# Kernel tuning notes

Hardware: AMD Instinct MI355X
Metric: run time of the kernel (lower is better)

## Reference

```python
import jax, jax.numpy as jnp
import numpy as np

NUM_NODE = 50000
NUM_EDGE = 1_600_000
NUM_REL = 512
DIM = 64


def setup_inputs() -> dict:
    key = jax.random.key(0)
    k1, k2, k3, k4, k5, k6 = jax.random.split(key, 6)
    inp = jax.random.normal(k1, (NUM_NODE, DIM), dtype=jnp.float32)
    boundary = jax.random.normal(k2, (NUM_NODE, DIM), dtype=jnp.float32)
    node_in = jax.random.randint(k3, (NUM_EDGE,), 0, NUM_NODE)
    node_out = jax.random.randint(k4, (NUM_EDGE,), 0, NUM_NODE)
    rel = jax.random.randint(k5, (NUM_EDGE,), 0, NUM_REL)
    edge_list = jnp.stack([node_in, node_out, rel], axis=1).astype(jnp.int32)
    edge_weight = jnp.ones((NUM_EDGE,), dtype=jnp.float32)
    relation_weight = jax.random.normal(k6, (NUM_REL, DIM), dtype=jnp.float32)
    W = jax.random.normal(jax.random.fold_in(key, 7), (DIM, DIM), dtype=jnp.float32) / np.sqrt(DIM)
    b = jnp.zeros((DIM,), dtype=jnp.float32)
    return {"input": inp, "boundary": boundary, "edge_list": edge_list,
            "edge_weight": edge_weight, "relation_weight": relation_weight,
            "W": W, "b": b}


def reference(input, boundary, edge_list, edge_weight, relation_weight, W, b):
    node_in = edge_list[:, 0]
    node_out = edge_list[:, 1]
    rel = edge_list[:, 2]
    # message: DistMult = x_src * r_e   [E, D]
    msg = input[node_in] * relation_weight[rel]
    msg = msg * edge_weight[:, None]
    # std aggregation: sum and sq_sum scatters, boundary acts as an extra self-message
    s = jax.ops.segment_sum(msg, node_out, num_segments=NUM_NODE) + boundary
    sq = jax.ops.segment_sum(msg * msg, node_out, num_segments=NUM_NODE) + boundary * boundary
    deg = jax.ops.segment_sum(jnp.ones_like(edge_weight), node_out, num_segments=NUM_NODE)
    deg1 = (deg + 1.0)[:, None]  # degree_out + 1 (boundary counted)
    update = jnp.sqrt(jnp.clip(sq / deg1 - (s / deg1) ** 2, 1e-6))
    # add_model: single Linear (MLP with num_mlp_layer=1, no trailing activation)
    return update @ W.T + b
```

## Files before the change

### kernel.cpp

```cpp
#include <hip/hip_runtime.h>
#include <hip/hip_bf16.h>

#define NN  50000
#define NE  1600000
#define DIM 64
#define NBK 391

#define OFF_FLAGS  0
#define OFF_BOFF   8
#define OFF_BCUR   400
#define OFF_ROWPTR 792
#define OFF_EIDX   50800

#define CHUNK 4096
#define SBCAP 8192

typedef __bf16 bf16x8 __attribute__((ext_vector_type(8)));
typedef __bf16 bf16x4 __attribute__((ext_vector_type(4)));
typedef float  f32x4  __attribute__((ext_vector_type(4)));

__device__ __forceinline__ float loadF(const void* p, int i, int bf) {
  if (bf) return __bfloat162float(((const __hip_bfloat16*)p)[i]);
  return ((const float*)p)[i];
}

__device__ __forceinline__ float4 loadF4(const void* p, int i4, int bf) {
  if (bf) {
    ushort4 u = ((const ushort4*)p)[i4];
    float4 f;
    union { unsigned int ui; float fl; } c;
    c.ui = (unsigned int)u.x << 16; f.x = c.fl;
    c.ui = (unsigned int)u.y << 16; f.y = c.fl;
    c.ui = (unsigned int)u.z << 16; f.z = c.fl;
    c.ui = (unsigned int)u.w << 16; f.w = c.fl;
    return f;
  }
  return ((const float4*)p)[i4];
}

__global__ void k_detect(const void* input, const void* boundary,
                         const void* relw, const void* W, const void* ew,
                         int* flags, int* boff) {
  __shared__ int cnt;
  int t = threadIdx.x;
  const void* arrs[4] = {input, boundary, relw, W};
  for (int a = 0; a < 4; ++a) {
    if (t == 0) cnt = 0;
    __syncthreads();
    const unsigned short* u = (const unsigned short*)arrs[a];
    unsigned ex = (u[2 * t] >> 7) & 0xFF;
    if (ex >= 100 && ex <= 140) atomicAdd(&cnt, 1);
    __syncthreads();
    if (t == 0) flags[a] = (cnt >= 32) ? 1 : 0;
    __syncthreads();
  }
  if (t == 0) {
    flags[4] = (((const unsigned short*)ew)[0] == 0x3F80) ? 1 : 0;
    flags[5] = 1;
  }
  for (int i = t; i < 392; i += 64) boff[i] = 0;
}

__global__ __launch_bounds__(256) void k_bhist(const int* __restrict__ el,
                                               const void* __restrict__ ew,
                                               int* __restrict__ bcnt,
                                               int* __restrict__ flags) {
  __shared__ int lc[NBK];
  int t = threadIdx.x;
  int bfE = flags[4];
  for (int i = t; i < NBK; i += 256) lc[i] = 0;
  __syncthreads();
  int c0 = blockIdx.x * 8192;
  int bad = 0;
  for (int i = t; i < 8192; i += 256) {
    int e = c0 + i;
    if (e < NE) {
      atomicAdd(&lc[el[e * 3 + 1] >> 7], 1);
      if (loadF(ew, e, bfE) != 1.0f) bad = 1;
    }
  }
  if (bad) flags[5] = 0;
  __syncthreads();
  for (int i = t; i < NBK; i += 256)
    if (lc[i]) atomicAdd(&bcnt[i], lc[i]);
}

__global__ __launch_bounds__(256) void k_scanb(int* __restrict__ boff,
                                               int* __restrict__ bcur,
                                               int* __restrict__ rowptr) {
  __shared__ int sc[256];
  int t = threadIdx.x;
  int i0 = 2 * t, i1 = 2 * t + 1;
  int a = (i0 < 392) ? boff[i0] : 0;
  int b = (i1 < 392) ? boff[i1] : 0;
  sc[t] = a + b;
  __syncthreads();
  for (int off = 1; off < 256; off <<= 1) {
    int v = (t >= off) ? sc[t - off] : 0;
    __syncthreads();
    sc[t] += v;
    __syncthreads();
  }
  int excl = sc[t] - (a + b);
  if (i0 < 392) boff[i0] = excl;
  if (i1 < 392) boff[i1] = excl + a;
  if (i0 < NBK) bcur[i0] = excl;
  if (i1 < NBK) bcur[i1] = excl + a;
  if (t == 255) rowptr[NN] = sc[255];
}

__global__ __launch_bounds__(256) void k_parta(
    const int* __restrict__ el, int* __restrict__ bcur,
    int* __restrict__ eidx, const int* __restrict__ flags,
    const int* __restrict__ boff, int gb0, int gb1, int cap) {
  __shared__ int stage[CHUNK];
  __shared__ unsigned short sbk[CHUNK];
  __shared__ int lh[NBK], lbase[NBK], lh2[NBK], gbs[NBK];
  __shared__ int sc[256];
  __shared__ int total;
  int t = threadIdx.x;
  int nb = gb1 - gb0;
  int c0 = blockIdx.x * CHUNK;
  int ones = flags[5];
  int base0 = boff[gb0];
  for (int i = t; i < nb; i += 256) { lh[i] = 0; lh2[i] = 0; }
  __syncthreads();
  for (int i = t; i < CHUNK; i += 256) {
    int e = c0 + i;
    if (e < NE) {
      int b = (el[e * 3 + 1] >> 7) - gb0;
      if (b >= 0 && b < nb) atomicAdd(&lh[b], 1);
    }
  }
  __syncthreads();
  int a0 = (2 * t < nb) ? lh[2 * t] : 0;
  int a1 = (2 * t + 1 < nb) ? lh[2 * t + 1] : 0;
  sc[t] = a0 + a1;
  __syncthreads();
  for (int off = 1; off < 256; off <<= 1) {
    int v = (t >= off) ? sc[t - off] : 0;
    __syncthreads();
    sc[t] += v;
    __syncthreads();
  }
  int excl = sc[t] - (a0 + a1);
  if (2 * t < nb) {
    lbase[2 * t] = excl;
    if (a0 > 0) gbs[2 * t] = atomicAdd(&bcur[gb0 + 2 * t], a0);
  }
  if (2 * t + 1 < nb) {
    lbase[2 * t + 1] = excl + a0;
    if (a1 > 0) gbs[2 * t + 1] = atomicAdd(&bcur[gb0 + 2 * t + 1], a1);
  }
  if (t == 255) total = sc[255];
  __syncthreads();
  for (int i = t; i < CHUNK; i += 256) {
    int e = c0 + i;
    if (e < NE) {
      int nout = el[e * 3 + 1];
      int b = (nout >> 7) - gb0;
      if (b >= 0 && b < nb) {
        int r = atomicAdd(&lh2[b], 1);
        int slot = lbase[b] + r;
        int rec = ones ? (el[e * 3] | (el[e * 3 + 2] << 16) |
                          ((nout & 127) << 25))
                       : (e | ((nout & 127) << 25));
        stage[slot] = rec;
        sbk[slot] = (unsigned short)b;
      }
    }
  }
  __syncthreads();
  int tot = total;
  for (int i = t; i < tot; i += 256) {
    int b = sbk[i];
    int dst = gbs[b] + (i - lbase[b]) - base0;
    if (dst >= 0 && dst < cap) eidx[dst] = stage[i];
  }
}

__global__ __launch_bounds__(256) void k_partb(
    int* __restrict__ eidx, const int* __restrict__ boff,
    int* __restrict__ rowptr, const int* __restrict__ el,
    const int* __restrict__ flags, int gb0, int cap) {
  __shared__ int ld[SBCAP];
  __shared__ int lcnt[128], lexc[128];
  int t = threadIdx.x;
  int b = gb0 + blockIdx.x;
  int n0 = b * 128;
  int ncnt = min(128, NN - n0);
  int base0 = boff[gb0];
  int rbase = boff[b], rend = boff[b + 1];
  int cnt = rend - rbase;
  int fast = (cnt <= SBCAP) && (rend - base0 <= cap);
  if (t < 128) lcnt[t] = 0;
  __syncthreads();
  if (fast) {
    for (int i = t; i < cnt; i += 256) ld[i] = eidx[rbase - base0 + i];
    __syncthreads();
    for (int i = t; i < cnt; i += 256)
      atomicAdd(&lcnt[(((unsigned)ld[i]) >> 25) & 127], 1);
  } else {
    int lim = n0 + ncnt;
    for (int e = t; e < NE; e += 256) {
      int nout = el[e * 3 + 1];
      if (nout >= n0 && nout < lim) atomicAdd(&lcnt[nout - n0], 1);
    }
  }
  __syncthreads();
  if (t < 128) lexc[t] = lcnt[t];
  __syncthreads();
  for (int off = 1; off < 128; off <<= 1) {
    int v = 0;
    if (t < 128 && t >= off) v = lexc[t - off];
    __syncthreads();
    if (t < 128) lexc[t] += v;
    __syncthreads();
  }
  if (t < 128) lexc[t] -= lcnt[t];
  __syncthreads();
  if (t < ncnt) rowptr[n0 + t] = rbase + lexc[t];
  if (t == 0) rowptr[n0 + ncnt] = rend;
  if (t < 128) lcnt[t] = 0;
  __syncthreads();
  if (fast) {
    for (int i = t; i < cnt; i += 256) {
      int rec = ld[i];
      int l = (((unsigned)rec) >> 25) & 127;
      int r = atomicAdd(&lcnt[l], 1);
      int dst = rbase + lexc[l] + r - base0;
      if (dst >= 0 && dst < cap) eidx[dst] = rec & 0x1FFFFFF;
    }
  } else {
    int ones = flags[5];
    int lim = n0 + ncnt;
    for (int e = t; e < NE; e += 256) {
      int nout = el[e * 3 + 1];
      if (nout >= n0 && nout < lim) {
        int l = nout - n0;
        int r = atomicAdd(&lcnt[l], 1);
        int dst = rbase + lexc[l] + r - base0;
        int rec = ones ? (el[e * 3] | (el[e * 3 + 2] << 16)) : e;
        if (dst >= 0 && dst < cap) eidx[dst] = rec;
      }
    }
  }
}

__global__ __launch_bounds__(256) void k_node(
    const void* __restrict__ input, const void* __restrict__ boundary,
    const int* __restrict__ el, const void* __restrict__ ew,
    const void* __restrict__ relw, const void* __restrict__ W,
    const void* __restrict__ bv, const int* __restrict__ rowptr,
    const int* __restrict__ eidx, const int* __restrict__ flags,
    void* __restrict__ out, int lo, int hi, int cap) {
  __shared__ __bf16 updb[16][72];

  int bfI = flags[0], bfB = flags[1], bfR = flags[2], bfW = flags[3],
      bfE = flags[4], ones = flags[5];
  int t  = threadIdx.x;
  int wv = t >> 6, ln = t & 63;
  int g  = ln >> 4;
  int k  = ln & 15;
  int q  = ln >> 4;
  int n0 = lo + blockIdx.x * 16;
  int base0 = rowptr[lo];

  int cc = wv * 16 + (ln & 15);
  bf16x8 bfr0, bfr1;
  #pragma unroll
  for (int j = 0; j < 8; ++j) {
    bfr0[j] = (__bf16)loadF(W, cc * 64 + q * 8 + j, bfW);
    bfr1[j] = (__bf16)loadF(W, cc * 64 + 32 + q * 8 + j, bfW);
  }
  float bias = loadF(bv, cc, bfW);

  const float4* inp4 = (const float4*)input;
  const float4* rw4  = (const float4*)relw;
  int hot = (!bfI && !bfR && ones) ? 1 : 0;

  for (int rr = 0; rr < 4; ++rr) {
    int row = wv * 4 + rr;
    int n = n0 + row;
    if (n >= hi) {
      updb[row][ln] = (__bf16)0.0f;
      continue;
    }
    int start = rowptr[n] - base0, end = rowptr[n + 1] - base0;
    int deg = end - start;
    float4 s4 = {0.f,0.f,0.f,0.f}, q4 = {0.f,0.f,0.f,0.f};
    if (hot) {
      for (int base = start; base < end; base += 64) {
        int mm = end - base; if (mm > 64) mm = 64;
        int rec = 0;
        int idx2 = base + ln;
        if (ln < mm && idx2 < cap) rec = eidx[idx2];
        int jmax = (mm + 3) >> 2;
        #pragma unroll 8
        for (int j = 0; j < jmax; ++j) {
          int slot = j * 4 + g;
          int pk = __shfl(rec, slot);
          float wsel = (slot < mm) ? 1.0f : 0.0f;
          int nin = pk & 0xFFFF, rl = (pk >> 16) & 0x1FF;
          float4 a = inp4[nin * 16 + k];
          float4 r = rw4[rl * 16 + k];
          float tx = a.x*r.x, ty = a.y*r.y, tz = a.z*r.z, tw = a.w*r.w;
          s4.x = fmaf(wsel, tx, s4.x); q4.x = fmaf(wsel, tx*tx, q4.x);
          s4.y = fmaf(wsel, ty, s4.y); q4.y = fmaf(wsel, ty*ty, q4.y);
          s4.z = fmaf(wsel, tz, s4.z); q4.z = fmaf(wsel, tz*tz, q4.z);
          s4.w = fmaf(wsel, tw, s4.w); q4.w = fmaf(wsel, tw*tw, q4.w);
        }
      }
    } else {
      for (int base = start; base < end; base += 64) {
        int mm = end - base; if (mm > 64) mm = 64;
        int rec = 0; float wrec = 0.0f;
        int idx2 = base + ln;
        if (ln < mm && idx2 < cap) {
          rec = eidx[idx2] & 0x1FFFFFF;
          if (!ones) wrec = loadF(ew, rec, bfE);
        }
        int jmax = (mm + 3) >> 2;
        for (int j = 0; j < jmax; ++j) {
          int slot = j * 4 + g;
          int rj = __shfl(rec, slot);
          int nin, rl; float wj;
          if (ones) { nin = rj & 0xFFFF; rl = (rj >> 16) & 0x1FF; wj = 1.0f; }
          else      { nin = el[rj * 3]; rl = el[rj * 3 + 2];
                      wj = __shfl(wrec, slot); }
          float wsel = (slot < mm) ? wj : 0.0f;
          float4 a = loadF4(input, nin * 16 + k, bfI);
          float4 r = loadF4(relw, rl * 16 + k, bfR);
          float tx = a.x*r.x, ty = a.y*r.y, tz = a.z*r.z, tw = a.w*r.w;
          s4.x = fmaf(wsel, tx, s4.x); q4.x = fmaf(wsel*tx, tx, q4.x);
          s4.y = fmaf(wsel, ty, s4.y); q4.y = fmaf(wsel*ty, ty, q4.y);
          s4.z = fmaf(wsel, tz, s4.z); q4.z = fmaf(wsel*tz, tz, q4.z);
          s4.w = fmaf(wsel, tw, s4.w); q4.w = fmaf(wsel*tw, tw, q4.w);
        }
      }
    }
    s4.x += __shfl_xor(s4.x, 16); s4.x += __shfl_xor(s4.x, 32);
    s4.y += __shfl_xor(s4.y, 16); s4.y += __shfl_xor(s4.y, 32);
    s4.z += __shfl_xor(s4.z, 16); s4.z += __shfl_xor(s4.z, 32);
    s4.w += __shfl_xor(s4.w, 16); s4.w += __shfl_xor(s4.w, 32);
    q4.x += __shfl_xor(q4.x, 16); q4.x += __shfl_xor(q4.x, 32);
    q4.y += __shfl_xor(q4.y, 16); q4.y += __shfl_xor(q4.y, 32);
    q4.z += __shfl_xor(q4.z, 16); q4.z += __shfl_xor(q4.z, 32);
    q4.w += __shfl_xor(q4.w, 16); q4.w += __shfl_xor(q4.w, 32);
    if (g == 0) {
      float4 b4 = loadF4(boundary, n * 16 + k, bfB);
      float dg = (float)deg + 1.0f;
      float sv, qv;
      bf16x4 u;
      sv = (s4.x + b4.x) / dg; qv = (q4.x + b4.x * b4.x) / dg;
      u[0] = (__bf16)sqrtf(fmaxf(qv - sv * sv, 1e-6f));
      sv = (s4.y + b4.y) / dg; qv = (q4.y + b4.y * b4.y) / dg;
      u[1] = (__bf16)sqrtf(fmaxf(qv - sv * sv, 1e-6f));
      sv = (s4.z + b4.z) / dg; qv = (q4.z + b4.z * b4.z) / dg;
      u[2] = (__bf16)sqrtf(fmaxf(qv - sv * sv, 1e-6f));
      sv = (s4.w + b4.w) / dg; qv = (q4.w + b4.w * b4.w) / dg;
      u[3] = (__bf16)sqrtf(fmaxf(qv - sv * sv, 1e-6f));
      *(bf16x4*)&updb[row][4 * k] = u;
    }
  }
  __syncthreads();

  bf16x8 af0 = *(const bf16x8*)&updb[ln & 15][q * 8];
  bf16x8 af1 = *(const bf16x8*)&updb[ln & 15][32 + q * 8];
  f32x4 acc = {0.f, 0.f, 0.f, 0.f};
  acc = __builtin_amdgcn_mfma_f32_16x16x32_bf16(af0, bfr0, acc, 0, 0, 0);
  acc = __builtin_amdgcn_mfma_f32_16x16x32_bf16(af1, bfr1, acc, 0, 0, 0);
  #pragma unroll
  for (int i = 0; i < 4; ++i) {
    int n = n0 + q * 4 + i;
    if (n < hi) {
      float v = acc[i] + bias;
      if (bfI) ((__hip_bfloat16*)out)[n * 64 + cc] = __float2bfloat16(v);
      else     ((float*)out)[n * 64 + cc] = v;
    }
  }
}

extern "C" void kernel_launch(void* const* d_in, const int* in_sizes, int n_in,
                              void* d_out, int out_size, void* d_ws, size_t ws_size,
                              hipStream_t stream) {
  const void* input    = d_in[0];
  const void* boundary = d_in[1];
  const int*  edges    = (const int*)d_in[2];
  const void* eweight  = d_in[3];
  const void* relw     = d_in[4];
  const void* W        = d_in[5];
  const void* bv       = d_in[6];

  int* wsI    = (int*)d_ws;
  int* flags  = wsI + OFF_FLAGS;
  int* boff   = wsI + OFF_BOFF;
  int* bcur   = wsI + OFF_BCUR;
  int* rowptr = wsI + OFF_ROWPTR;
  int* eidx   = wsI + OFF_EIDX;

  long cap = (long)(ws_size / 4) - OFF_EIDX;
  if (cap < 1) cap = 1;
  int npass;
  if      (cap >= (long)NE) npass = 1;
  else if (cap >= 1000000)  npass = 2;
  else if (cap >= 520000)   npass = 4;
  else                      npass = 8;

  k_detect<<<1, 64, 0, stream>>>(input, boundary, relw, W, eweight,
                                 flags, boff);
  k_bhist<<<(NE + 8191) / 8192, 256, 0, stream>>>(edges, eweight, boff, flags);
  k_scanb<<<1, 256, 0, stream>>>(boff, bcur, rowptr);

  const int PA_NB = (NE + CHUNK - 1) / CHUNK;
  for (int p = 0; p < npass; ++p) {
    int gb0 = NBK * p / npass;
    int gb1 = NBK * (p + 1) / npass;
    int lo = gb0 * 128;
    int hi = (gb1 * 128 < NN) ? gb1 * 128 : NN;
    k_parta<<<PA_NB, 256, 0, stream>>>(edges, bcur, eidx, flags, boff,
                                       gb0, gb1, (int)cap);
    k_partb<<<gb1 - gb0, 256, 0, stream>>>(eidx, boff, rowptr, edges, flags,
                                           gb0, (int)cap);
    k_node<<<(hi - lo + 15) / 16, 256, 0, stream>>>(
        input, boundary, edges, eweight, relw, W, bv, rowptr, eidx, flags,
        d_out, lo, hi, (int)cap);
  }
}
```

Before: 245.8 us.

## Replace two-level bucket partition with per-node histogram, scan, and atomic scatter

Drops the bucketed two-stage CSR build (bucket histogram, LDS-staged partition, then a per-bucket local sort). It builds the CSR with a per-node global atomic histogram, a three-kernel multi-block prefix scan, and a direct scatter using per-node global atomic cursors. This removes the LDS staging and the second pass over the edge records, but it adds contention on global atomics and produces uncoalesced scattered writes. Edge order within each node's row becomes nondeterministic.

Result: slower. 331.9 us (+35.0%).

```diff
diff --git a/kernel.cpp b/kernel.cpp
--- a/kernel.cpp
+++ b/kernel.cpp
@@ -4,16 +4,12 @@
 #define NN  50000
 #define NE  1600000
 #define DIM 64
-#define NBK 391
 
 #define OFF_FLAGS  0
-#define OFF_BOFF   8
-#define OFF_BCUR   400
-#define OFF_ROWPTR 792
-#define OFF_EIDX   50800
-
-#define CHUNK 4096
-#define SBCAP 8192
+#define OFF_ROWPTR 8
+#define OFF_CUR    50016
+#define OFF_PART   100016
+#define OFF_EIDX   100096
 
 typedef __bf16 bf16x8 __attribute__((ext_vector_type(8)));
 typedef __bf16 bf16x4 __attribute__((ext_vector_type(4)));
@@ -40,7 +36,7 @@
 
 __global__ void k_detect(const void* input, const void* boundary,
                          const void* relw, const void* W, const void* ew,
-                         int* flags, int* boff) {
+                         int* flags) {
   __shared__ int cnt;
   int t = threadIdx.x;
   const void* arrs[4] = {input, boundary, relw, W};
@@ -58,189 +54,108 @@
     flags[4] = (((const unsigned short*)ew)[0] == 0x3F80) ? 1 : 0;
     flags[5] = 1;
   }
-  for (int i = t; i < 392; i += 64) boff[i] = 0;
-}
-
-__global__ __launch_bounds__(256) void k_bhist(const int* __restrict__ el,
-                                               const void* __restrict__ ew,
-                                               int* __restrict__ bcnt,
-                                               int* __restrict__ flags) {
-  __shared__ int lc[NBK];
-  int t = threadIdx.x;
+}
+
+__global__ __launch_bounds__(256) void k_zero(int* __restrict__ rowptr) {
+  int i0 = (blockIdx.x * 256 + threadIdx.x) * 4;
+  #pragma unroll
+  for (int j = 0; j < 4; ++j) {
+    int i = i0 + j;
+    if (i <= NN) rowptr[i] = 0;
+  }
+}
+
+__global__ __launch_bounds__(256) void k_hist(const int* __restrict__ el,
+                                              const void* __restrict__ ew,
+                                              int* __restrict__ rowptr,
+                                              int* __restrict__ flags) {
   int bfE = flags[4];
-  for (int i = t; i < NBK; i += 256) lc[i] = 0;
-  __syncthreads();
   int c0 = blockIdx.x * 8192;
   int bad = 0;
-  for (int i = t; i < 8192; i += 256) {
+  for (int i = threadIdx.x; i < 8192; i += 256) {
     int e = c0 + i;
     if (e < NE) {
-      atomicAdd(&lc[el[e * 3 + 1] >> 7], 1);
+      atomicAdd(&rowptr[el[e * 3 + 1]], 1);
       if (loadF(ew, e, bfE) != 1.0f) bad = 1;
     }
   }
   if (bad) flags[5] = 0;
-  __syncthreads();
-  for (int i = t; i < NBK; i += 256)
-    if (lc[i]) atomicAdd(&bcnt[i], lc[i]);
-}
-
-__global__ __launch_bounds__(256) void k_scanb(int* __restrict__ boff,
-                                               int* __restrict__ bcur,
-                                               int* __restrict__ rowptr) {
+}
+
+__global__ __launch_bounds__(256) void k_scan1(int* __restrict__ rowptr,
+                                               int* __restrict__ part) {
   __shared__ int sc[256];
   int t = threadIdx.x;
-  int i0 = 2 * t, i1 = 2 * t + 1;
-  int a = (i0 < 392) ? boff[i0] : 0;
-  int b = (i1 < 392) ? boff[i1] : 0;
-  sc[t] = a + b;
+  int base = blockIdx.x * 1024 + t * 4;
+  int v[4]; int s = 0;
+  #pragma unroll
+  for (int j = 0; j < 4; ++j) {
+    int idx = base + j;
+    v[j] = (idx < NN) ? rowptr[idx] : 0;
+    s += v[j];
+  }
+  sc[t] = s;
   __syncthreads();
   for (int off = 1; off < 256; off <<= 1) {
-    int v = (t >= off) ? sc[t - off] : 0;
-    __syncthreads();
-    sc[t] += v;
-    __syncthreads();
-  }
-  int excl = sc[t] - (a + b);
-  if (i0 < 392) boff[i0] = excl;
-  if (i1 < 392) boff[i1] = excl + a;
-  if (i0 < NBK) bcur[i0] = excl;
-  if (i1 < NBK) bcur[i1] = excl + a;
-  if (t == 255) rowptr[NN] = sc[255];
-}
-
-__global__ __launch_bounds__(256) void k_parta(
-    const int* __restrict__ el, int* __restrict__ bcur,
+    int x = (t >= off) ? sc[t - off] : 0;
+    __syncthreads();
+    sc[t] += x;
+    __syncthreads();
+  }
+  int excl = sc[t] - s;
+  #pragma unroll
+  for (int j = 0; j < 4; ++j) {
+    int idx = base + j;
+    if (idx < NN) rowptr[idx] = excl;
+    excl += v[j];
+  }
+  if (t == 255) part[blockIdx.x] = sc[255];
+}
+
+__global__ void k_scan2(int* __restrict__ part, int* __restrict__ rowptr) {
+  int t = threadIdx.x;
+  int v = (t < 49) ? part[t] : 0;
+  int orig = v;
+  #pragma unroll
+  for (int d = 1; d < 64; d <<= 1) {
+    int u = __shfl_up(v, d);
+    if (t >= d) v += u;
+  }
+  if (t < 49) part[t] = v - orig;
+  if (t == 0) rowptr[NN] = NE;
+}
+
+__global__ __launch_bounds__(256) void k_scan3(int* __restrict__ rowptr,
+                                               const int* __restrict__ part,
+                                               int* __restrict__ cur) {
+  int off = part[blockIdx.x];
+  int base = blockIdx.x * 1024 + threadIdx.x * 4;
+  #pragma unroll
+  for (int j = 0; j < 4; ++j) {
+    int idx = base + j;
+    if (idx < NN) {
+      int a = rowptr[idx] + off;
+      rowptr[idx] = a;
+      cur[idx] = a;
+    }
+  }
+}
+
+__global__ __launch_bounds__(256) void k_scatter(
+    const int* __restrict__ el, int* __restrict__ cur,
     int* __restrict__ eidx, const int* __restrict__ flags,
-    const int* __restrict__ boff, int gb0, int gb1, int cap) {
-  __shared__ int stage[CHUNK];
-  __shared__ unsigned short sbk[CHUNK];
-  __shared__ int lh[NBK], lbase[NBK], lh2[NBK], gbs[NBK];
-  __shared__ int sc[256];
-  __shared__ int total;
-  int t = threadIdx.x;
-  int nb = gb1 - gb0;
-  int c0 = blockIdx.x * CHUNK;
+    const int* __restrict__ rowptr, int lo, int hi, int cap) {
   int ones = flags[5];
-  int base0 = boff[gb0];
-  for (int i = t; i < nb; i += 256) { lh[i] = 0; lh2[i] = 0; }
-  __syncthreads();
-  for (int i = t; i < CHUNK; i += 256) {
-    int e = c0 + i;
-    if (e < NE) {
-      int b = (el[e * 3 + 1] >> 7) - gb0;
-      if (b >= 0 && b < nb) atomicAdd(&lh[b], 1);
-    }
-  }
-  __syncthreads();
-  int a0 = (2 * t < nb) ? lh[2 * t] : 0;
-  int a1 = (2 * t + 1 < nb) ? lh[2 * t + 1] : 0;
-  sc[t] = a0 + a1;
-  __syncthreads();
-  for (int off = 1; off < 256; off <<= 1) {
-    int v = (t >= off) ? sc[t - off] : 0;
-    __syncthreads();
-    sc[t] += v;
-    __syncthreads();
-  }
-  int excl = sc[t] - (a0 + a1);
-  if (2 * t < nb) {
-    lbase[2 * t] = excl;
-    if (a0 > 0) gbs[2 * t] = atomicAdd(&bcur[gb0 + 2 * t], a0);
-  }
-  if (2 * t + 1 < nb) {
-    lbase[2 * t + 1] = excl + a0;
-    if (a1 > 0) gbs[2 * t + 1] = atomicAdd(&bcur[gb0 + 2 * t + 1], a1);
-  }
-  if (t == 255) total = sc[255];
-  __syncthreads();
-  for (int i = t; i < CHUNK; i += 256) {
+  int base0 = rowptr[lo];
+  int c0 = blockIdx.x * 8192;
+  for (int i = threadIdx.x; i < 8192; i += 256) {
     int e = c0 + i;
     if (e < NE) {
       int nout = el[e * 3 + 1];
-      int b = (nout >> 7) - gb0;
-      if (b >= 0 && b < nb) {
-        int r = atomicAdd(&lh2[b], 1);
-        int slot = lbase[b] + r;
-        int rec = ones ? (el[e * 3] | (el[e * 3 + 2] << 16) |
-                          ((nout & 127) << 25))
-                       : (e | ((nout & 127) << 25));
-        stage[slot] = rec;
-        sbk[slot] = (unsigned short)b;
-      }
-    }
-  }
-  __syncthreads();
-  int tot = total;
-  for (int i = t; i < tot; i += 256) {
-    int b = sbk[i];
-    int dst = gbs[b] + (i - lbase[b]) - base0;
-    if (dst >= 0 && dst < cap) eidx[dst] = stage[i];
-  }
-}
-
-__global__ __launch_bounds__(256) void k_partb(
-    int* __restrict__ eidx, const int* __restrict__ boff,
-    int* __restrict__ rowptr, const int* __restrict__ el,
-    const int* __restrict__ flags, int gb0, int cap) {
-  __shared__ int ld[SBCAP];
-  __shared__ int lcnt[128], lexc[128];
-  int t = threadIdx.x;
-  int b = gb0 + blockIdx.x;
-  int n0 = b * 128;
-  int ncnt = min(128, NN - n0);
-  int base0 = boff[gb0];
-  int rbase = boff[b], rend = boff[b + 1];
-  int cnt = rend - rbase;
-  int fast = (cnt <= SBCAP) && (rend - base0 <= cap);
-  if (t < 128) lcnt[t] = 0;
-  __syncthreads();
-  if (fast) {
-    for (int i = t; i < cnt; i += 256) ld[i] = eidx[rbase - base0 + i];
-    __syncthreads();
-    for (int i = t; i < cnt; i += 256)
-      atomicAdd(&lcnt[(((unsigned)ld[i]) >> 25) & 127], 1);
-  } else {
-    int lim = n0 + ncnt;
-    for (int e = t; e < NE; e += 256) {
-      int nout = el[e * 3 + 1];
-      if (nout >= n0 && nout < lim) atomicAdd(&lcnt[nout - n0], 1);
-    }
-  }
-  __syncthreads();
-  if (t < 128) lexc[t] = lcnt[t];
-  __syncthreads();
-  for (int off = 1; off < 128; off <<= 1) {
-    int v = 0;
-    if (t < 128 && t >= off) v = lexc[t - off];
-    __syncthreads();
-    if (t < 128) lexc[t] += v;
-    __syncthreads();
-  }
-  if (t < 128) lexc[t] -= lcnt[t];
-  __syncthreads();
-  if (t < ncnt) rowptr[n0 + t] = rbase + lexc[t];
-  if (t == 0) rowptr[n0 + ncnt] = rend;
-  if (t < 128) lcnt[t] = 0;
-  __syncthreads();
-  if (fast) {
-    for (int i = t; i < cnt; i += 256) {
-      int rec = ld[i];
-      int l = (((unsigned)rec) >> 25) & 127;
-      int r = atomicAdd(&lcnt[l], 1);
-      int dst = rbase + lexc[l] + r - base0;
-      if (dst >= 0 && dst < cap) eidx[dst] = rec & 0x1FFFFFF;
-    }
-  } else {
-    int ones = flags[5];
-    int lim = n0 + ncnt;
-    for (int e = t; e < NE; e += 256) {
-      int nout = el[e * 3 + 1];
-      if (nout >= n0 && nout < lim) {
-        int l = nout - n0;
-        int r = atomicAdd(&lcnt[l], 1);
-        int dst = rbase + lexc[l] + r - base0;
+      if (nout >= lo && nout < hi) {
+        int r = atomicAdd(&cur[nout], 1);
         int rec = ones ? (el[e * 3] | (el[e * 3 + 2] << 16)) : e;
+        int dst = r - base0;
         if (dst >= 0 && dst < cap) eidx[dst] = rec;
       }
     }
@@ -394,9 +309,9 @@
 
   int* wsI    = (int*)d_ws;
   int* flags  = wsI + OFF_FLAGS;
-  int* boff   = wsI + OFF_BOFF;
-  int* bcur   = wsI + OFF_BCUR;
   int* rowptr = wsI + OFF_ROWPTR;
+  int* cur    = wsI + OFF_CUR;
+  int* part   = wsI + OFF_PART;
   int* eidx   = wsI + OFF_EIDX;
 
   long cap = (long)(ws_size / 4) - OFF_EIDX;
@@ -407,21 +322,18 @@
   else if (cap >= 520000)   npass = 4;
   else                      npass = 8;
 
-  k_detect<<<1, 64, 0, stream>>>(input, boundary, relw, W, eweight,
-                                 flags, boff);
-  k_bhist<<<(NE + 8191) / 8192, 256, 0, stream>>>(edges, eweight, boff, flags);
-  k_scanb<<<1, 256, 0, stream>>>(boff, bcur, rowptr);
-
-  const int PA_NB = (NE + CHUNK - 1) / CHUNK;
+  k_detect<<<1, 64, 0, stream>>>(input, boundary, relw, W, eweight, flags);
+  k_zero<<<49, 256, 0, stream>>>(rowptr);
+  k_hist<<<(NE + 8191) / 8192, 256, 0, stream>>>(edges, eweight, rowptr, flags);
+  k_scan1<<<49, 256, 0, stream>>>(rowptr, part);
+  k_scan2<<<1, 64, 0, stream>>>(part, rowptr);
+  k_scan3<<<49, 256, 0, stream>>>(rowptr, part, cur);
+
   for (int p = 0; p < npass; ++p) {
-    int gb0 = NBK * p / npass;
-    int gb1 = NBK * (p + 1) / npass;
-    int lo = gb0 * 128;
-    int hi = (gb1 * 128 < NN) ? gb1 * 128 : NN;
-    k_parta<<<PA_NB, 256, 0, stream>>>(edges, bcur, eidx, flags, boff,
-                                       gb0, gb1, (int)cap);
-    k_partb<<<gb1 - gb0, 256, 0, stream>>>(eidx, boff, rowptr, edges, flags,
-                                           gb0, (int)cap);
+    int lo = (int)((long)NN * p / npass);
+    int hi = (int)((long)NN * (p + 1) / npass);
+    k_scatter<<<(NE + 8191) / 8192, 256, 0, stream>>>(
+        edges, cur, eidx, flags, rowptr, lo, hi, (int)cap);
     k_node<<<(hi - lo + 15) / 16, 256, 0, stream>>>(
         input, boundary, edges, eweight, relw, W, bv, rowptr, eidx, flags,
         d_out, lo, hi, (int)cap);
```

## Stage input and relation weights as fp16 for gather, unroll edge loop

Applied to the files above, without the earlier changes.

Adds a staging kernel that converts the node features and relation weights to fp16 in workspace. The hot gather path in the node kernel then reads half as many bytes per edge, cutting the memory traffic of the random gathers. The edge loop is manually unrolled by four so more loads are in flight, and a masked tail handles leftover edges. Launch bounds are raised for occupancy and the partition chunk size is halved. The trade-off is reduced input precision, an extra conversion pass and more workspace use, which can shrink the eidx capacity.

Measured after the change: 259.5 us. +5.6%, slower.

```diff
diff --git a/kernel.cpp b/kernel.cpp
--- a/kernel.cpp
+++ b/kernel.cpp
@@ -1,5 +1,6 @@
 #include <hip/hip_runtime.h>
 #include <hip/hip_bf16.h>
+#include <hip/hip_fp16.h>
 
 #define NN  50000
 #define NE  1600000
@@ -10,9 +11,11 @@
 #define OFF_BOFF   8
 #define OFF_BCUR   400
 #define OFF_ROWPTR 792
-#define OFF_EIDX   50800
-
-#define CHUNK 4096
+#define OFF_INP16  50800
+#define OFF_RELW16 1650800
+#define OFF_EIDX_H 1667184
+
+#define CHUNK 2048
 #define SBCAP 8192
 
 typedef __bf16 bf16x8 __attribute__((ext_vector_type(8)));
@@ -38,6 +41,25 @@
   return ((const float4*)p)[i4];
 }
 
+__device__ __forceinline__ float4 h4f(ushort4 u) {
+  float4 f;
+  f.x = __half2float(__ushort_as_half(u.x));
+  f.y = __half2float(__ushort_as_half(u.y));
+  f.z = __half2float(__ushort_as_half(u.z));
+  f.w = __half2float(__ushort_as_half(u.w));
+  return f;
+}
+
+__device__ __forceinline__ void accum(ushort4 ua, ushort4 ur,
+                                      float4& s4, float4& q4) {
+  float4 a = h4f(ua), r = h4f(ur);
+  float tx = a.x * r.x, ty = a.y * r.y, tz = a.z * r.z, tw = a.w * r.w;
+  s4.x += tx; q4.x = fmaf(tx, tx, q4.x);
+  s4.y += ty; q4.y = fmaf(ty, ty, q4.y);
+  s4.z += tz; q4.z = fmaf(tz, tz, q4.z);
+  s4.w += tw; q4.w = fmaf(tw, tw, q4.w);
+}
+
 __global__ void k_detect(const void* input, const void* boundary,
                          const void* relw, const void* W, const void* ew,
                          int* flags, int* boff) {
@@ -59,6 +81,33 @@
     flags[5] = 1;
   }
   for (int i = t; i < 392; i += 64) boff[i] = 0;
+}
+
+__global__ __launch_bounds__(256) void k_stage(const void* __restrict__ in,
+                                               const void* __restrict__ rw,
+                                               unsigned short* __restrict__ inph,
+                                               unsigned short* __restrict__ rwh,
+                                               const int* __restrict__ flags) {
+  if (flags[0] || flags[2]) return;
+  int i = blockIdx.x * 256 + threadIdx.x;
+  if (i < NN * 16) {
+    float4 v = ((const float4*)in)[i];
+    ushort4 h;
+    h.x = __half_as_ushort(__float2half(v.x));
+    h.y = __half_as_ushort(__float2half(v.y));
+    h.z = __half_as_ushort(__float2half(v.z));
+    h.w = __half_as_ushort(__float2half(v.w));
+    ((ushort4*)inph)[i] = h;
+  }
+  if (i < 512 * 16) {
+    float4 v = ((const float4*)rw)[i];
+    ushort4 h;
+    h.x = __half_as_ushort(__float2half(v.x));
+    h.y = __half_as_ushort(__float2half(v.y));
+    h.z = __half_as_ushort(__float2half(v.z));
+    h.w = __half_as_ushort(__float2half(v.w));
+    ((ushort4*)rwh)[i] = h;
+  }
 }
 
 __global__ __launch_bounds__(256) void k_bhist(const int* __restrict__ el,
@@ -247,12 +296,14 @@
   }
 }
 
-__global__ __launch_bounds__(256) void k_node(
+__global__ __launch_bounds__(256, 4) void k_node(
     const void* __restrict__ input, const void* __restrict__ boundary,
     const int* __restrict__ el, const void* __restrict__ ew,
     const void* __restrict__ relw, const void* __restrict__ W,
     const void* __restrict__ bv, const int* __restrict__ rowptr,
     const int* __restrict__ eidx, const int* __restrict__ flags,
+    const unsigned short* __restrict__ inph,
+    const unsigned short* __restrict__ rwh,
     void* __restrict__ out, int lo, int hi, int cap) {
   __shared__ __bf16 updb[16][72];
 
@@ -275,9 +326,10 @@
   }
   float bias = loadF(bv, cc, bfW);
 
-  const float4* inp4 = (const float4*)input;
-  const float4* rw4  = (const float4*)relw;
+  const ushort4* ih4 = (const ushort4*)inph;
+  const ushort4* rh4 = (const ushort4*)rwh;
   int hot = (!bfI && !bfR && ones) ? 1 : 0;
+  int hotH = hot && (inph != 0);
 
   for (int rr = 0; rr < 4; ++rr) {
     int row = wv * 4 + rr;
@@ -289,26 +341,51 @@
     int start = rowptr[n] - base0, end = rowptr[n + 1] - base0;
     int deg = end - start;
     float4 s4 = {0.f,0.f,0.f,0.f}, q4 = {0.f,0.f,0.f,0.f};
-    if (hot) {
+    if (hotH) {
       for (int base = start; base < end; base += 64) {
         int mm = end - base; if (mm > 64) mm = 64;
         int rec = 0;
         int idx2 = base + ln;
         if (ln < mm && idx2 < cap) rec = eidx[idx2];
+        int jq = mm >> 2;
         int jmax = (mm + 3) >> 2;
-        #pragma unroll 8
-        for (int j = 0; j < jmax; ++j) {
+        int j = 0;
+        for (; j + 4 <= jq; j += 4) {
+          int pk0 = __shfl(rec, j * 4 + g);
+          int pk1 = __shfl(rec, j * 4 + 4 + g);
+          int pk2 = __shfl(rec, j * 4 + 8 + g);
+          int pk3 = __shfl(rec, j * 4 + 12 + g);
+          ushort4 a0 = ih4[(pk0 & 0xFFFF) * 16 + k];
+          ushort4 r0 = rh4[((pk0 >> 16) & 0x1FF) * 16 + k];
+          ushort4 a1 = ih4[(pk1 & 0xFFFF) * 16 + k];
+          ushort4 r1 = rh4[((pk1 >> 16) & 0x1FF) * 16 + k];
+          ushort4 a2 = ih4[(pk2 & 0xFFFF) * 16 + k];
+          ushort4 r2 = rh4[((pk2 >> 16) & 0x1FF) * 16 + k];
+          ushort4 a3 = ih4[(pk3 & 0xFFFF) * 16 + k];
+          ushort4 r3 = rh4[((pk3 >> 16) & 0x1FF) * 16 + k];
+          accum(a0, r0, s4, q4);
+          accum(a1, r1, s4, q4);
+          accum(a2, r2, s4, q4);
+          accum(a3, r3, s4, q4);
+        }
+        for (; j < jq; ++j) {
+          int pk = __shfl(rec, j * 4 + g);
+          ushort4 a = ih4[(pk & 0xFFFF) * 16 + k];
+          ushort4 r = rh4[((pk >> 16) & 0x1FF) * 16 + k];
+          accum(a, r, s4, q4);
+        }
+        for (; j < jmax; ++j) {
           int slot = j * 4 + g;
-          int pk = __shfl(rec, slot);
+          int pk = __shfl(rec, slot & 63);
           float wsel = (slot < mm) ? 1.0f : 0.0f;
-          int nin = pk & 0xFFFF, rl = (pk >> 16) & 0x1FF;
-          float4 a = inp4[nin * 16 + k];
-          float4 r = rw4[rl * 16 + k];
+          ushort4 ua = ih4[(pk & 0xFFFF) * 16 + k];
+          ushort4 ur = rh4[((pk >> 16) & 0x1FF) * 16 + k];
+          float4 a = h4f(ua), r = h4f(ur);
           float tx = a.x*r.x, ty = a.y*r.y, tz = a.z*r.z, tw = a.w*r.w;
-          s4.x = fmaf(wsel, tx, s4.x); q4.x = fmaf(wsel, tx*tx, q4.x);
-          s4.y = fmaf(wsel, ty, s4.y); q4.y = fmaf(wsel, ty*ty, q4.y);
-          s4.z = fmaf(wsel, tz, s4.z); q4.z = fmaf(wsel, tz*tz, q4.z);
-          s4.w = fmaf(wsel, tw, s4.w); q4.w = fmaf(wsel, tw*tw, q4.w);
+          s4.x = fmaf(wsel, tx, s4.x); q4.x = fmaf(wsel*tx, tx, q4.x);
+          s4.y = fmaf(wsel, ty, s4.y); q4.y = fmaf(wsel*ty, ty, q4.y);
+          s4.z = fmaf(wsel, tz, s4.z); q4.z = fmaf(wsel*tz, tz, q4.z);
+          s4.w = fmaf(wsel, tw, s4.w); q4.w = fmaf(wsel*tw, tw, q4.w);
         }
       }
     } else {
@@ -397,9 +474,13 @@
   int* boff   = wsI + OFF_BOFF;
   int* bcur   = wsI + OFF_BCUR;
   int* rowptr = wsI + OFF_ROWPTR;
-  int* eidx   = wsI + OFF_EIDX;
-
-  long cap = (long)(ws_size / 4) - OFF_EIDX;
+
+  long avail = (long)(ws_size / 4) - OFF_INP16;
+  int useH = (avail >= (long)NE + 1600000 + 16384) ? 1 : 0;
+  unsigned short* inph = useH ? (unsigned short*)(wsI + OFF_INP16) : 0;
+  unsigned short* rwh  = useH ? (unsigned short*)(wsI + OFF_RELW16) : 0;
+  int* eidx = useH ? (wsI + OFF_EIDX_H) : (wsI + OFF_INP16);
+  long cap = useH ? (avail - 1600000 - 16384) : avail;
   if (cap < 1) cap = 1;
   int npass;
   if      (cap >= (long)NE) npass = 1;
@@ -409,6 +490,9 @@
 
   k_detect<<<1, 64, 0, stream>>>(input, boundary, relw, W, eweight,
                                  flags, boff);
+  if (useH)
+    k_stage<<<(NN * 16 + 255) / 256, 256, 0, stream>>>(input, relw, inph,
+                                                       rwh, flags);
   k_bhist<<<(NE + 8191) / 8192, 256, 0, stream>>>(edges, eweight, boff, flags);
   k_scanb<<<1, 256, 0, stream>>>(boff, bcur, rowptr);
 
@@ -424,6 +508,6 @@
                                            gb0, (int)cap);
     k_node<<<(hi - lo + 15) / 16, 256, 0, stream>>>(
         input, boundary, edges, eweight, relw, W, bv, rowptr, eidx, flags,
-        d_out, lo, hi, (int)cap);
-  }
-}
+        inph, rwh, d_out, lo, hi, (int)cap);
+  }
+}
```
